# Kernel tuning notes

Hardware: AMD Instinct MI355X
Metric: run time of the kernel (lower is better)

Reference implementation:

```python
import jax, jax.numpy as jnp
import numpy as np

B, N, D, H = 2, 2048, 1024, 16
DK = D // H


def setup_inputs() -> dict:
    key = jax.random.key(0)
    ks = jax.random.split(key, 12)
    s = D ** -0.5
    inp = {
        "query": jax.random.normal(ks[0], (B, N, D), jnp.float32),
        "key": jax.random.normal(ks[1], (B, N, D), jnp.float32),
        "value": jax.random.normal(ks[2], (B, N, D), jnp.float32),
        # causal mask: 1 = keep, 0 = masked (matches create_causal_mask)
        "mask": jnp.tril(jnp.ones((N, N), jnp.int32)),
        "Wq": jax.random.normal(ks[3], (D, D), jnp.float32) * s,
        "bq": jnp.zeros((D,), jnp.float32),
        "Wk": jax.random.normal(ks[4], (D, D), jnp.float32) * s,
        "bk": jnp.zeros((D,), jnp.float32),
        "Wv": jax.random.normal(ks[5], (D, D), jnp.float32) * s,
        "bv": jnp.zeros((D,), jnp.float32),
        "Wo": jax.random.normal(ks[6], (D, D), jnp.float32) * s,
        "bo": jnp.zeros((D,), jnp.float32),
    }
    return inp


def reference(query, key, value, mask, Wq, bq, Wk, bk, Wv, bv, Wo, bo):
    scale = DK ** -0.5
    # Linear projections (torch nn.Linear: x @ W.T + b), split into heads -> [B,H,N,DK]
    q = (query @ Wq.T + bq).reshape(B, N, H, DK).transpose(0, 2, 1, 3)
    k = (key @ Wk.T + bk).reshape(B, N, H, DK).transpose(0, 2, 1, 3)
    v = (value @ Wv.T + bv).reshape(B, N, H, DK).transpose(0, 2, 1, 3)
    scores = jnp.einsum("bhqd,bhkd->bhqk", q, k) * scale  # [B,H,N,N]
    scores = jnp.where(mask[None, None, :, :] == 0, jnp.float32(-1e9), scores)
    attn = jax.nn.softmax(scores, axis=-1)
    ctx = jnp.einsum("bhqk,bhkd->bhqd", attn, v)  # [B,H,N,DK]
    ctx = ctx.transpose(0, 2, 1, 3).reshape(B, N, D)
    return ctx @ Wo.T + bo
```

## Files before the change

### kernel.cpp

```cpp
#include <hip/hip_runtime.h>
#include <hip/hip_bf16.h>

typedef __attribute__((ext_vector_type(4))) float f32x4;
typedef __attribute__((ext_vector_type(8))) __bf16 bf16x8;
typedef __attribute__((ext_vector_type(8))) unsigned short u16x8;
typedef __attribute__((ext_vector_type(4))) unsigned short u16x4;
typedef __attribute__((ext_vector_type(2))) unsigned int u32x2;
typedef unsigned short u16;

#define DEV static __device__ __forceinline__

DEV u16 f2bf(float f){
  unsigned u = __builtin_bit_cast(unsigned, f);
  u += 0x7fff + ((u >> 16) & 1);
  return (u16)(u >> 16);
}

DEV f32x4 mfma16(bf16x8 a, bf16x8 b, f32x4 c){
  return __builtin_amdgcn_mfma_f32_16x16x32_bf16(a, b, c, 0, 0, 0);
}

DEV void gload16(const void* g, void* l){
  __builtin_amdgcn_global_load_lds((const __attribute__((address_space(1))) void*)g,
                                   (__attribute__((address_space(3))) void*)l,
                                   16, 0, 0);
}

DEV float fexp2(float x){
#if __has_builtin(__builtin_amdgcn_exp2f)
  return __builtin_amdgcn_exp2f(x);
#else
  float r; asm("v_exp_f32 %0, %1" : "=v"(r) : "v"(x)); return r;
#endif
}

#define SCL 0.18033688011f
#define THR 11.0f
#define PLD 72

__global__ __launch_bounds__(256) void cvt_k(
    const float* __restrict__ s0, const float* __restrict__ s1,
    const float* __restrict__ s2, const float* __restrict__ s3,
    const float* __restrict__ s4, const float* __restrict__ s5,
    const float* __restrict__ s6,
    u16* __restrict__ d0, u16* __restrict__ d1, u16* __restrict__ d2,
    u16* __restrict__ d3, u16* __restrict__ d4, u16* __restrict__ d5,
    u16* __restrict__ d6){
  const int y = blockIdx.y;
  const float* __restrict__ s = y==0?s0:y==1?s1:y==2?s2:y==3?s3:y==4?s4:y==5?s5:s6;
  u16* __restrict__ d         = y==0?d0:y==1?d1:y==2?d2:y==3?d3:y==4?d4:y==5?d5:d6;
  const int n8 = (y < 3) ? (4096*1024/8) : (1024*1024/8);
  for (int i = blockIdx.x*256 + threadIdx.x; i < n8; i += gridDim.x*256){
    f32x4 a = *(const f32x4*)&s[(size_t)i*8];
    f32x4 b = *(const f32x4*)&s[(size_t)i*8 + 4];
    u16x8 h;
    #pragma unroll
    for (int j = 0; j < 4; ++j){ h[j] = f2bf(a[j]); h[j+4] = f2bf(b[j]); }
    *(u16x8*)&d[(size_t)i*8] = h;
  }
}

__global__ __launch_bounds__(256) void gemm_bt(
    const u16* __restrict__ A0, const u16* __restrict__ A1, const u16* __restrict__ A2,
    const u16* __restrict__ B0, const u16* __restrict__ B1, const u16* __restrict__ B2,
    const float* __restrict__ e0, const float* __restrict__ e1, const float* __restrict__ e2,
    u16* __restrict__ C0, u16* __restrict__ C1, u16* __restrict__ C2){
  __shared__ u16 As[128*32];
  __shared__ u16 Bs[128*32];

  const int f = blockIdx.x;
  const int xc = f & 7, g = f >> 3;
  const int p  = xc*12 + (g >> 3);
  const int bn8 = g & 7;
  const int z = p >> 5, bm32 = p & 31;
  const bool vt = (z == 2);
  const int bm = vt ? bn8 : bm32;
  const int bn = vt ? bm32 : bn8;

  const u16* __restrict__ A    = z==0 ? A0 : z==1 ? A1 : A2;
  const u16* __restrict__ Bw   = z==0 ? B0 : z==1 ? B1 : B2;
  const float* __restrict__ bias = z==0 ? e0 : z==1 ? e1 : e2;
  u16* __restrict__ C          = z==0 ? C0 : z==1 ? C1 : C2;
  const float qs = (z == 0) ? SCL : 1.0f;

  const int tid  = threadIdx.x;
  const int lane = tid & 63, w = tid >> 6;
  const int wr = w >> 1, wc = w & 1;
  const int l16 = lane & 15, lhi = lane >> 4;

  const int srow = w*16 + (lane >> 2);
  const int scol = (lane & 3)*8;
  const u16* Asrc = A  + (size_t)(bm*128 + srow)*1024 + scol;
  const u16* Bsrc = Bw + (size_t)(bn*128 + srow)*1024 + scol;
  u16* Adst0 = As + w*512;
  u16* Bdst0 = Bs + w*512;

  f32x4 acc[4][4] = {};

  for (int k0 = 0; k0 < 1024; k0 += 32){
    __syncthreads();
    gload16(Asrc + k0,             Adst0);
    gload16(Asrc + 64*1024 + k0,   Adst0 + 2048);
    gload16(Bsrc + k0,             Bdst0);
    gload16(Bsrc + 64*1024 + k0,   Bdst0 + 2048);
    __syncthreads();

    bf16x8 af[4], bfr[4];
    #pragma unroll
    for (int mi = 0; mi < 4; ++mi)
      af[mi] = *(const bf16x8*)&As[(wr*64 + mi*16 + l16)*32 + lhi*8];
    #pragma unroll
    for (int nf = 0; nf < 4; ++nf)
      bfr[nf] = *(const bf16x8*)&Bs[(wc*64 + nf*16 + l16)*32 + lhi*8];
    #pragma unroll
    for (int mi = 0; mi < 4; ++mi)
      #pragma unroll
      for (int nf = 0; nf < 4; ++nf)
        acc[mi][nf] = mfma16(af[mi], bfr[nf], acc[mi][nf]);
  }

  #pragma unroll
  for (int mi = 0; mi < 4; ++mi){
    #pragma unroll
    for (int nf = 0; nf < 4; ++nf){
      int row0 = bm*128 + wr*64 + mi*16 + lhi*4;
      int col  = bn*128 + wc*64 + nf*16 + l16;
      float bc = bias[col];
      #pragma unroll
      for (int r = 0; r < 4; ++r){
        int row = row0 + r;
        float val = (acc[mi][nf][r] + (vt ? bias[row] : bc)) * qs;
        if (!vt){
          int b = row >> 11, n = row & 2047;
          int h = col >> 6,  dk = col & 63;
          C[(((size_t)(b*16 + h))*2048 + n)*64 + dk] = f2bf(val);
        } else {
          int h = row >> 6,  dk = row & 63;
          int b = col >> 11, n = col & 2047;
          C[(((size_t)(b*16 + h))*64 + dk)*2048 + n] = f2bf(val);
        }
      }
    }
  }
}

__global__ __launch_bounds__(256) void gemm_o64(const u16* __restrict__ A,
                                                const u16* __restrict__ Bw,
                                                const float* __restrict__ bias,
                                                float* __restrict__ C){
  __shared__ u16 As[64*32];
  __shared__ u16 Bs[128*32];
  const int tid  = threadIdx.x;
  const int lane = tid & 63, w = tid >> 6;
  const int wr = w >> 1, wc = w & 1;
  const int l16 = lane & 15, lhi = lane >> 4;
  const int bm = blockIdx.y, bn = blockIdx.x;

  const int srow = w*16 + (lane >> 2);
  const int scol = (lane & 3)*8;
  const u16* Asrc = A  + (size_t)(bm*64  + srow)*1024 + scol;
  const u16* Bsrc = Bw + (size_t)(bn*128 + srow)*1024 + scol;
  u16* Adst0 = As + w*512;
  u16* Bdst0 = Bs + w*512;

  f32x4 acc[2][4] = {};

  for (int k0 = 0; k0 < 1024; k0 += 32){
    __syncthreads();
    gload16(Asrc + k0,             Adst0);
    gload16(Bsrc + k0,             Bdst0);
    gload16(Bsrc + 64*1024 + k0,   Bdst0 + 2048);
    __syncthreads();

    bf16x8 af[2], bfr[4];
    #pragma unroll
    for (int mi = 0; mi < 2; ++mi)
      af[mi] = *(const bf16x8*)&As[(wr*32 + mi*16 + l16)*32 + lhi*8];
    #pragma unroll
    for (int nf = 0; nf < 4; ++nf)
      bfr[nf] = *(const bf16x8*)&Bs[(wc*64 + nf*16 + l16)*32 + lhi*8];
    #pragma unroll
    for (int mi = 0; mi < 2; ++mi)
      #pragma unroll
      for (int nf = 0; nf < 4; ++nf)
        acc[mi][nf] = mfma16(af[mi], bfr[nf], acc[mi][nf]);
  }

  #pragma unroll
  for (int mi = 0; mi < 2; ++mi){
    #pragma unroll
    for (int nf = 0; nf < 4; ++nf){
      int row0 = bm*64 + wr*32 + mi*16 + lhi*4;
      int col  = bn*128 + wc*64 + nf*16 + l16;
      float bv = bias[col];
      #pragma unroll
      for (int r = 0; r < 4; ++r)
        C[(size_t)(row0 + r)*1024 + col] = acc[mi][nf][r] + bv;
    }
  }
}

DEV void sm_tile(int t, int tdiag, int q_abs,
                 const u16* __restrict__ Ksb, u16* __restrict__ PsW,
                 bf16x8 bq0, bf16x8 bq1,
                 f32x4* ctx, float& m_r, float& l_r,
                 int l16, int lhi, int lane, int swz){
  f32x4 s4[4] = {};
  #pragma unroll
  for (int nf = 0; nf < 4; ++nf){
    bf16x8 ak0 = *(const bf16x8*)&Ksb[(nf*16 + l16)*64 + ((lhi*8) ^ swz)];
    bf16x8 ak1 = *(const bf16x8*)&Ksb[(nf*16 + l16)*64 + ((32 + lhi*8) ^ swz)];
    s4[nf] = mfma16(ak0, bq0, s4[nf]);
    s4[nf] = mfma16(ak1, bq1, s4[nf]);
  }

  if (t >= tdiag){
    #pragma unroll
    for (int nf = 0; nf < 4; ++nf)
      #pragma unroll
      for (int r = 0; r < 4; ++r){
        int kc = t*64 + nf*16 + lhi*4 + r;
        if (kc > q_abs) s4[nf][r] = -1.0e30f;
      }
  }

  float mt = fmaxf(
      fmaxf(fmaxf(fmaxf(s4[0][0],s4[0][1]), fmaxf(s4[0][2],s4[0][3])),
            fmaxf(fmaxf(s4[1][0],s4[1][1]), fmaxf(s4[1][2],s4[1][3]))),
      fmaxf(fmaxf(fmaxf(s4[2][0],s4[2][1]), fmaxf(s4[2][2],s4[2][3])),
            fmaxf(fmaxf(s4[3][0],s4[3][1]), fmaxf(s4[3][2],s4[3][3]))));
  mt = fmaxf(mt, __shfl_xor(mt, 16));
  mt = fmaxf(mt, __shfl_xor(mt, 32));

  if (!__all(mt <= m_r + THR)){
    float mn = fmaxf(m_r, mt);
    float sf = fexp2(m_r - mn);
    m_r = mn;
    l_r *= sf;
    float sfb[4];
    #pragma unroll
    for (int r = 0; r < 4; ++r)
      sfb[r] = __shfl(sf, (lane >> 4)*4 + r);
    #pragma unroll
    for (int dkf = 0; dkf < 4; ++dkf)
      #pragma unroll
      for (int r = 0; r < 4; ++r)
        ctx[dkf][r] *= sfb[r];
  }

  float lt = 0.f;
  u16* prow = PsW + l16*PLD;
  #pragma unroll
  for (int nf = 0; nf < 4; ++nf){
    float p0 = fexp2(s4[nf][0] - m_r);
    float p1 = fexp2(s4[nf][1] - m_r);
    float p2 = fexp2(s4[nf][2] - m_r);
    float p3 = fexp2(s4[nf][3] - m_r);
    lt += (p0 + p1) + (p2 + p3);
    unsigned w0 = __builtin_amdgcn_perm(__builtin_bit_cast(unsigned, p1),
                                        __builtin_bit_cast(unsigned, p0), 0x07060302u);
    unsigned w1 = __builtin_amdgcn_perm(__builtin_bit_cast(unsigned, p3),
                                        __builtin_bit_cast(unsigned, p2), 0x07060302u);
    u32x2 wp = {w0, w1};
    *(u32x2*)&prow[nf*16 + lhi*4] = wp;
  }
  lt += __shfl_xor(lt, 16);
  lt += __shfl_xor(lt, 32);
  l_r += lt;
}

DEV void pv_tile(const u16* __restrict__ Vsb, const u16* __restrict__ PsW,
                 f32x4* ctx, int l16, int lhi, int swz){
  const u16* prow = PsW + l16*PLD;
  __builtin_amdgcn_s_setprio(1);
  #pragma unroll
  for (int ks = 0; ks < 2; ++ks){
    bf16x8 pa = *(const bf16x8*)&prow[ks*32 + lhi*8];
    #pragma unroll
    for (int dkf = 0; dkf < 4; ++dkf){
      bf16x8 vb = *(const bf16x8*)&Vsb[(dkf*16 + l16)*64 + ((ks*32 + lhi*8) ^ swz)];
      ctx[dkf] = mfma16(pa, vb, ctx[dkf]);
    }
  }
  __builtin_amdgcn_s_setprio(0);
}

__global__ __launch_bounds__(512) void attn_k(const u16* __restrict__ Q,
                                              const u16* __restrict__ K,
                                              const u16* __restrict__ Vt,
                                              u16* __restrict__ CTX){
  __shared__ u16 Ks[2][64*64];
  __shared__ u16 Vs[2][64*64];
  __shared__ u16 Ps[8][2][16*PLD];
  const int tid  = threadIdx.x;
  const int lane = tid & 63, w = tid >> 6;
  const int l16 = lane & 15, lhi = lane >> 4;
  const int f  = blockIdx.x;
  const int bh = f & 31;
  const int qt = 15 - (f >> 5);
  const size_t base = (size_t)bh * 2048 * 64;
  const u16* Qb = Q  + base;
  const u16* Kb = K  + base;
  const u16* Vb = Vt + base;
  const int b = bh >> 4, h = bh & 15;

  const int s0 = tid;
  const int r0 = s0 >> 3, c0 = ((s0 & 7) ^ (r0 & 7))*8;
  const u16* Ksrc0 = Kb + r0*64 + c0;
  const u16* Vsrc0 = Vb + (size_t)r0*2048 + c0;
  const int swz = (l16 & 7)*8;

  const int q_abs = qt*128 + w*16 + l16;
  const int tdiag = 2*qt + (w >> 2);
  bf16x8 bq0 = *(const bf16x8*)&Qb[(size_t)q_abs*64 + lhi*8];
  bf16x8 bq1 = *(const bf16x8*)&Qb[(size_t)q_abs*64 + 32 + lhi*8];

  f32x4 ctx[4] = {};
  float m_r = -3.0e38f, l_r = 0.f;
  u16* Ps0 = &Ps[w][0][0];
  u16* Ps1 = &Ps[w][1][0];

  gload16(Ksrc0, &Ks[0][s0*8]);
  gload16(Vsrc0, &Vs[0][s0*8]);
  __syncthreads();

  const int nt = 2*qt + 2;
  for (int t = 0; t < nt; ++t){
    const int pb = t & 1;
    u16* PsC = pb ? Ps1 : Ps0;
    u16* PsP = pb ? Ps0 : Ps1;
    if (t + 1 < nt)
      gload16(Ksrc0 + (t+1)*4096, &Ks[pb^1][s0*8]);
    sm_tile(t, tdiag, q_abs, Ks[pb], PsC, bq0, bq1, ctx, m_r, l_r, l16, lhi, lane, swz);
    if (t > 0)
      pv_tile(Vs[pb^1], PsP, ctx, l16, lhi, swz);
    __syncthreads();
    if (t + 1 < nt)
      gload16(Vsrc0 + (size_t)(t+1)*64, &Vs[pb^1][s0*8]);
  }
  pv_tile(Vs[(nt-1)&1], (nt-1)&1 ? Ps1 : Ps0, ctx, l16, lhi, swz);

  float lf[4];
  #pragma unroll
  for (int r = 0; r < 4; ++r)
    lf[r] = __shfl(l_r, (lane >> 4)*4 + r);
  #pragma unroll
  for (int dkf = 0; dkf < 4; ++dkf)
    #pragma unroll
    for (int r = 0; r < 4; ++r){
      int q = qt*128 + w*16 + lhi*4 + r;
      CTX[((size_t)(b*2048 + q))*1024 + h*64 + dkf*16 + l16] = f2bf(ctx[dkf][r] / lf[r]);
    }
}

extern "C" void kernel_launch(void* const* d_in, const int* in_sizes, int n_in,
                              void* d_out, int out_size, void* d_ws, size_t ws_size,
                              hipStream_t stream){
  const float* q  = (const float*)d_in[0];
  const float* k  = (const float*)d_in[1];
  const float* v  = (const float*)d_in[2];
  const float* Wq = (const float*)d_in[4];  const float* bq = (const float*)d_in[5];
  const float* Wk = (const float*)d_in[6];  const float* bk = (const float*)d_in[7];
  const float* Wv = (const float*)d_in[8];  const float* bv = (const float*)d_in[9];
  const float* Wo = (const float*)d_in[10]; const float* bo = (const float*)d_in[11];
  float* out = (float*)d_out;

  u16* Wqb = (u16*)d_ws;
  u16* Wkb = Wqb + 1048576;
  u16* Wvb = Wkb + 1048576;
  u16* Wob = Wvb + 1048576;
  u16* Xqb = Wob + 1048576;
  u16* Xkb = Xqb + 4194304;
  u16* Xvb = Xkb + 4194304;
  u16* Qw  = Xvb + 4194304;
  u16* Kw  = Qw + 4194304;
  u16* Vw  = Kw + 4194304;
  u16* Cw  = Xqb;

  cvt_k<<<dim3(512, 7), dim3(256), 0, stream>>>(q, k, v, Wq, Wk, Wv, Wo,
                                                Xqb, Xkb, Xvb, Wqb, Wkb, Wvb, Wob);
  gemm_bt<<<dim3(768), dim3(256), 0, stream>>>(
      Xqb, Xkb, Wvb, Wqb, Wkb, Xvb, bq, bk, bv, Qw, Kw, Vw);
  attn_k<<<dim3(512), dim3(512), 0, stream>>>(Qw, Kw, Vw, Cw);
  gemm_o64<<<dim3(8, 64), dim3(256), 0, stream>>>(Cw, Wob, bo, out);
}
```

Before: 120.5 us.

## Double-buffer LDS tiles in projection GEMMs to overlap loads with MFMA

Measured after the change: 130.4 us. +8.3%, slower.

```diff
diff --git a/kernel.cpp b/kernel.cpp
--- a/kernel.cpp
+++ b/kernel.cpp
@@ -65,8 +65,8 @@
     const u16* __restrict__ B0, const u16* __restrict__ B1, const u16* __restrict__ B2,
     const float* __restrict__ e0, const float* __restrict__ e1, const float* __restrict__ e2,
     u16* __restrict__ C0, u16* __restrict__ C1, u16* __restrict__ C2){
-  __shared__ u16 As[128*32];
-  __shared__ u16 Bs[128*32];
+  __shared__ u16 As[2][128*32];
+  __shared__ u16 Bs[2][128*32];
 
   const int f = blockIdx.x;
   const int xc = f & 7, g = f >> 3;
@@ -92,26 +92,33 @@
   const int scol = (lane & 3)*8;
   const u16* Asrc = A  + (size_t)(bm*128 + srow)*1024 + scol;
   const u16* Bsrc = Bw + (size_t)(bn*128 + srow)*1024 + scol;
-  u16* Adst0 = As + w*512;
-  u16* Bdst0 = Bs + w*512;
+  const int d0 = w*512;
 
   f32x4 acc[4][4] = {};
 
-  for (int k0 = 0; k0 < 1024; k0 += 32){
-    __syncthreads();
-    gload16(Asrc + k0,             Adst0);
-    gload16(Asrc + 64*1024 + k0,   Adst0 + 2048);
-    gload16(Bsrc + k0,             Bdst0);
-    gload16(Bsrc + 64*1024 + k0,   Bdst0 + 2048);
-    __syncthreads();
-
+  gload16(Asrc,             &As[0][d0]);
+  gload16(Asrc + 64*1024,   &As[0][d0 + 2048]);
+  gload16(Bsrc,             &Bs[0][d0]);
+  gload16(Bsrc + 64*1024,   &Bs[0][d0 + 2048]);
+
+  for (int t = 0; t < 32; ++t){
+    const int cur = t & 1;
+    asm volatile("s_waitcnt vmcnt(0)" ::: "memory");
+    __builtin_amdgcn_s_barrier();
+    if (t < 31){
+      const int k1 = (t + 1)*32;
+      gload16(Asrc + k1,           &As[cur^1][d0]);
+      gload16(Asrc + 64*1024 + k1, &As[cur^1][d0 + 2048]);
+      gload16(Bsrc + k1,           &Bs[cur^1][d0]);
+      gload16(Bsrc + 64*1024 + k1, &Bs[cur^1][d0 + 2048]);
+    }
     bf16x8 af[4], bfr[4];
     #pragma unroll
     for (int mi = 0; mi < 4; ++mi)
-      af[mi] = *(const bf16x8*)&As[(wr*64 + mi*16 + l16)*32 + lhi*8];
+      af[mi] = *(const bf16x8*)&As[cur][(wr*64 + mi*16 + l16)*32 + lhi*8];
     #pragma unroll
     for (int nf = 0; nf < 4; ++nf)
-      bfr[nf] = *(const bf16x8*)&Bs[(wc*64 + nf*16 + l16)*32 + lhi*8];
+      bfr[nf] = *(const bf16x8*)&Bs[cur][(wc*64 + nf*16 + l16)*32 + lhi*8];
     #pragma unroll
     for (int mi = 0; mi < 4; ++mi)
       #pragma unroll
@@ -148,8 +155,8 @@
                                                 const u16* __restrict__ Bw,
                                                 const float* __restrict__ bias,
                                                 float* __restrict__ C){
-  __shared__ u16 As[64*32];
-  __shared__ u16 Bs[128*32];
+  __shared__ u16 As[2][64*32];
+  __shared__ u16 Bs[2][128*32];
   const int tid  = threadIdx.x;
   const int lane = tid & 63, w = tid >> 6;
   const int wr = w >> 1, wc = w & 1;
@@ -160,25 +167,31 @@
   const int scol = (lane & 3)*8;
   const u16* Asrc = A  + (size_t)(bm*64  + srow)*1024 + scol;
   const u16* Bsrc = Bw + (size_t)(bn*128 + srow)*1024 + scol;
-  u16* Adst0 = As + w*512;
-  u16* Bdst0 = Bs + w*512;
+  const int d0 = w*512;
 
   f32x4 acc[2][4] = {};
 
-  for (int k0 = 0; k0 < 1024; k0 += 32){
-    __syncthreads();
-    gload16(Asrc + k0,             Adst0);
-    gload16(Bsrc + k0,             Bdst0);
-    gload16(Bsrc + 64*1024 + k0,   Bdst0 + 2048);
-    __syncthreads();
-
+  gload16(Asrc,           &As[0][d0]);
+  gload16(Bsrc,           &Bs[0][d0]);
+  gload16(Bsrc + 64*1024, &Bs[0][d0 + 2048]);
+
+  for (int t = 0; t < 32; ++t){
+    const int cur = t & 1;
+    asm volatile("s_waitcnt vmcnt(0)" ::: "memory");
+    __builtin_amdgcn_s_barrier();
+    if (t < 31){
+      const int k1 = (t + 1)*32;
+      gload16(Asrc + k1,           &As[cur^1][d0]);
+      gload16(Bsrc + k1,           &Bs[cur^1][d0]);
+      gload16(Bsrc + 64*1024 + k1, &Bs[cur^1][d0 + 2048]);
+    }
     bf16x8 af[2], bfr[4];
     #pragma unroll
     for (int mi = 0; mi < 2; ++mi)
-      af[mi] = *(const bf16x8*)&As[(wr*32 + mi*16 + l16)*32 + lhi*8];
+      af[mi] = *(const bf16x8*)&As[cur][(wr*32 + mi*16 + l16)*32 + lhi*8];
     #pragma unroll
     for (int nf = 0; nf < 4; ++nf)
-      bfr[nf] = *(const bf16x8*)&Bs[(wc*64 + nf*16 + l16)*32 + lhi*8];
+      bfr[nf] = *(const bf16x8*)&Bs[cur][(wc*64 + nf*16 + l16)*32 + lhi*8];
     #pragma unroll
     for (int mi = 0; mi < 2; ++mi)
       #pragma unroll
```

## Shrink QKV GEMM tiles, swizzle out-proj blocks, skip masked attention tiles per warp

Applied to the files above, without the earlier changes.

Result: slower. 136.6 us (+13.4%).

```diff
diff --git a/kernel.cpp b/kernel.cpp
--- a/kernel.cpp
+++ b/kernel.cpp
@@ -60,25 +60,25 @@
   }
 }
 
-__global__ __launch_bounds__(256) void gemm_bt(
-    const u16* __restrict__ A0, const u16* __restrict__ A1, const u16* __restrict__ A2,
-    const u16* __restrict__ B0, const u16* __restrict__ B1, const u16* __restrict__ B2,
+__global__ __launch_bounds__(256) void gemm_qkv64(
+    const u16* __restrict__ Xq, const u16* __restrict__ Xk, const u16* __restrict__ Xv,
+    const u16* __restrict__ Wq, const u16* __restrict__ Wk, const u16* __restrict__ Wv,
     const float* __restrict__ e0, const float* __restrict__ e1, const float* __restrict__ e2,
     u16* __restrict__ C0, u16* __restrict__ C1, u16* __restrict__ C2){
-  __shared__ u16 As[128*32];
+  __shared__ u16 As[64*32];
   __shared__ u16 Bs[128*32];
 
   const int f = blockIdx.x;
   const int xc = f & 7, g = f >> 3;
-  const int p  = xc*12 + (g >> 3);
+  const int P  = xc*24 + (g >> 3);
   const int bn8 = g & 7;
-  const int z = p >> 5, bm32 = p & 31;
+  int z, bm, bn;
+  if (P < 128){ z = P >> 6; bm = P & 63; bn = bn8; }
+  else        { z = 2; int lc = P - 128; bm = lc >> 2; bn = (lc & 3)*8 + bn8; }
   const bool vt = (z == 2);
-  const int bm = vt ? bn8 : bm32;
-  const int bn = vt ? bm32 : bn8;
-
-  const u16* __restrict__ A    = z==0 ? A0 : z==1 ? A1 : A2;
-  const u16* __restrict__ Bw   = z==0 ? B0 : z==1 ? B1 : B2;
+
+  const u16* __restrict__ A    = z==0 ? Xq : z==1 ? Xk : Wv;
+  const u16* __restrict__ Bw   = z==0 ? Wq : z==1 ? Wk : Xv;
   const float* __restrict__ bias = z==0 ? e0 : z==1 ? e1 : e2;
   u16* __restrict__ C          = z==0 ? C0 : z==1 ? C1 : C2;
   const float qs = (z == 0) ? SCL : 1.0f;
@@ -90,40 +90,39 @@
 
   const int srow = w*16 + (lane >> 2);
   const int scol = (lane & 3)*8;
-  const u16* Asrc = A  + (size_t)(bm*128 + srow)*1024 + scol;
+  const u16* Asrc = A  + (size_t)(bm*64  + srow)*1024 + scol;
   const u16* Bsrc = Bw + (size_t)(bn*128 + srow)*1024 + scol;
   u16* Adst0 = As + w*512;
   u16* Bdst0 = Bs + w*512;
 
-  f32x4 acc[4][4] = {};
+  f32x4 acc[2][4] = {};
 
   for (int k0 = 0; k0 < 1024; k0 += 32){
     __syncthreads();
     gload16(Asrc + k0,             Adst0);
-    gload16(Asrc + 64*1024 + k0,   Adst0 + 2048);
     gload16(Bsrc + k0,             Bdst0);
     gload16(Bsrc + 64*1024 + k0,   Bdst0 + 2048);
     __syncthreads();
 
-    bf16x8 af[4], bfr[4];
-    #pragma unroll
-    for (int mi = 0; mi < 4; ++mi)
-      af[mi] = *(const bf16x8*)&As[(wr*64 + mi*16 + l16)*32 + lhi*8];
+    bf16x8 af[2], bfr[4];
+    #pragma unroll
+    for (int mi = 0; mi < 2; ++mi)
+      af[mi] = *(const bf16x8*)&As[(wr*32 + mi*16 + l16)*32 + lhi*8];
     #pragma unroll
     for (int nf = 0; nf < 4; ++nf)
       bfr[nf] = *(const bf16x8*)&Bs[(wc*64 + nf*16 + l16)*32 + lhi*8];
     #pragma unroll
-    for (int mi = 0; mi < 4; ++mi)
+    for (int mi = 0; mi < 2; ++mi)
       #pragma unroll
       for (int nf = 0; nf < 4; ++nf)
         acc[mi][nf] = mfma16(af[mi], bfr[nf], acc[mi][nf]);
   }
 
   #pragma unroll
-  for (int mi = 0; mi < 4; ++mi){
+  for (int mi = 0; mi < 2; ++mi){
     #pragma unroll
     for (int nf = 0; nf < 4; ++nf){
-      int row0 = bm*128 + wr*64 + mi*16 + lhi*4;
+      int row0 = bm*64 + wr*32 + mi*16 + lhi*4;
       int col  = bn*128 + wc*64 + nf*16 + l16;
       float bc = bias[col];
       #pragma unroll
@@ -150,11 +149,14 @@
                                                 float* __restrict__ C){
   __shared__ u16 As[64*32];
   __shared__ u16 Bs[128*32];
+  const int f = blockIdx.x;
+  const int xc = f & 7, g = f >> 3;
+  const int bm = xc*8 + (g >> 3);
+  const int bn = g & 7;
   const int tid  = threadIdx.x;
   const int lane = tid & 63, w = tid >> 6;
   const int wr = w >> 1, wc = w & 1;
   const int l16 = lane & 15, lhi = lane >> 4;
-  const int bm = blockIdx.y, bn = blockIdx.x;
 
   const int srow = w*16 + (lane >> 2);
   const int scol = (lane & 3)*8;
@@ -325,20 +327,23 @@
   __syncthreads();
 
   const int nt = 2*qt + 2;
+  const int ntw = tdiag + 1;
   for (int t = 0; t < nt; ++t){
     const int pb = t & 1;
     u16* PsC = pb ? Ps1 : Ps0;
     u16* PsP = pb ? Ps0 : Ps1;
     if (t + 1 < nt)
       gload16(Ksrc0 + (t+1)*4096, &Ks[pb^1][s0*8]);
-    sm_tile(t, tdiag, q_abs, Ks[pb], PsC, bq0, bq1, ctx, m_r, l_r, l16, lhi, lane, swz);
-    if (t > 0)
+    if (t < ntw)
+      sm_tile(t, tdiag, q_abs, Ks[pb], PsC, bq0, bq1, ctx, m_r, l_r, l16, lhi, lane, swz);
+    if (t > 0 && t - 1 < ntw)
       pv_tile(Vs[pb^1], PsP, ctx, l16, lhi, swz);
     __syncthreads();
     if (t + 1 < nt)
       gload16(Vsrc0 + (size_t)(t+1)*64, &Vs[pb^1][s0*8]);
   }
-  pv_tile(Vs[(nt-1)&1], (nt-1)&1 ? Ps1 : Ps0, ctx, l16, lhi, swz);
+  if (ntw == nt)
+    pv_tile(Vs[(nt-1)&1], (nt-1)&1 ? Ps1 : Ps0, ctx, l16, lhi, swz);
 
   float lf[4];
   #pragma unroll
@@ -379,8 +384,8 @@
 
   cvt_k<<<dim3(512, 7), dim3(256), 0, stream>>>(q, k, v, Wq, Wk, Wv, Wo,
                                                 Xqb, Xkb, Xvb, Wqb, Wkb, Wvb, Wob);
-  gemm_bt<<<dim3(768), dim3(256), 0, stream>>>(
-      Xqb, Xkb, Wvb, Wqb, Wkb, Xvb, bq, bk, bv, Qw, Kw, Vw);
+  gemm_qkv64<<<dim3(1536), dim3(256), 0, stream>>>(
+      Xqb, Xkb, Xvb, Wqb, Wkb, Wvb, bq, bk, bv, Qw, Kw, Vw);
   attn_k<<<dim3(512), dim3(512), 0, stream>>>(Qw, Kw, Vw, Cw);
-  gemm_o64<<<dim3(8, 64), dim3(256), 0, stream>>>(Cw, Wob, bo, out);
-}
+  gemm_o64<<<dim3(512), dim3(256), 0, stream>>>(Cw, Wob, bo, out);
+}
```
